# Kernel optimization log

Hardware: AMD Instinct MI355X
Metric: run time of the kernel (lower is better)

The kernel has to match this reference:

```python
import jax, jax.numpy as jnp
import numpy as np

B, DIM, HID = 16384, 1024, 2048
HALF = DIM // 2
# alternating checkerboard mask: even indices are 'masked' (conditioning) dims
_MASK = np.arange(DIM) % 2 == 0
MASK_IDX = np.nonzero(_MASK)[0]      # dims fed to the MLP (static)
NEG_IDX = np.nonzero(~_MASK)[0]      # dims transformed by the affine coupling (static)


def setup_inputs() -> dict:
    key = jax.random.key(0)
    ks = jax.random.split(key, 8)
    s = 0.02  # small init so exp(s) stays well-behaved
    return {
        "z": jax.random.normal(ks[0], (B, DIM), jnp.float32),
        "log_det": jnp.zeros((B,), jnp.float32),
        "W1": jax.random.normal(ks[1], (HID, HALF), jnp.float32) * s,
        "b1": jax.random.normal(ks[2], (HID,), jnp.float32) * s,
        "W2": jax.random.normal(ks[3], (HID, HID), jnp.float32) * s,
        "b2": jax.random.normal(ks[4], (HID,), jnp.float32) * s,
        "W3": jax.random.normal(ks[5], (DIM, HID), jnp.float32) * s,
        "b3": jax.random.normal(ks[6], (DIM,), jnp.float32) * s,
    }


def reference(z, log_det, W1, b1, W2, b2, W3, b3):
    # gather conditioning dims (static column indices -> jit-friendly)
    zm = z[:, MASK_IDX]                                    # [B, HALF]
    # 3-layer MLP with exact (erf) GELU, matching torch nn.GELU default
    h = jax.nn.gelu(zm @ W1.T + b1, approximate=False)     # [B, HID]
    h = jax.nn.gelu(h @ W2.T + b2, approximate=False)      # [B, HID]
    s_t = h @ W3.T + b3                                    # [B, DIM]
    s, t = s_t[:, :HALF], s_t[:, HALF:]                    # each [B, HALF]
    # affine coupling on the complementary dims, scatter back (forward, inverse=False)
    z_out = z.at[:, NEG_IDX].set(z[:, NEG_IDX] * jnp.exp(s) + t)
    log_det_out = log_det + jnp.sum(s, axis=1)
    return z_out, log_det_out
```

## Files before the change

kernel.cpp:

```cpp
#include <hip/hip_runtime.h>
#include <hip/hip_bf16.h>
#include <cstdint>

typedef __bf16 bf16x8 __attribute__((ext_vector_type(8)));
typedef float  f32x4  __attribute__((ext_vector_type(4)));

struct alignas(4) us2 { unsigned short x, y; };
struct alignas(8) us4 { unsigned short x, y, z, w; };

__device__ __forceinline__ unsigned short f2bf(float f) {
    union { float f; unsigned u; } a; a.f = f;
    unsigned r = a.u + 0x7fffu + ((a.u >> 16) & 1u);
    return (unsigned short)(r >> 16);
}

__device__ __forceinline__ void gl_lds16(const void* g, void* s) {
    __builtin_amdgcn_global_load_lds(
        (const __attribute__((address_space(1))) void*)g,
        (__attribute__((address_space(3))) void*)s, 16, 0, 0);
}

#define SCHEDB()  __builtin_amdgcn_sched_barrier(0)
#define SBAR()    do { SCHEDB(); __builtin_amdgcn_s_barrier(); SCHEDB(); } while (0)
#define WAITLG(N) do { asm volatile("s_waitcnt lgkmcnt(" #N ")" ::: "memory"); SCHEDB(); } while (0)
#define WAITVM(N) do { asm volatile("s_waitcnt vmcnt(" #N ")" ::: "memory"); SCHEDB(); } while (0)

template<int EPI, int K, int N>
__global__ __launch_bounds__(512, 2)
void gemm256(const unsigned short* __restrict__ A,
             const unsigned short* __restrict__ W,
             const float* __restrict__ bias,
             unsigned short* __restrict__ outb,
             float* __restrict__ outf,
             const float* __restrict__ zin,
             float* __restrict__ ldout)
{
    extern __shared__ char smem[];
    constexpr int NH = K / 32;
    constexpr int GX = N / 256;
    static_assert(NH % 2 == 0, "ping-pong unroll");

    const int tid  = threadIdx.x;
    const int lane = tid & 63;
    const int wv   = tid >> 6;
    const int wr   = wv >> 2, wc = wv & 3;

    const int bid = blockIdx.y * GX + blockIdx.x;
    const int nwg = GX * (int)gridDim.y;
    const int swz = (bid & 7) * (nwg >> 3) + (bid >> 3);
    const size_t row0 = (size_t)(swz / GX) * 256;
    const size_t col0 = (size_t)(swz % GX) * 256;

    const int cse = (((tid & 3) ^ ((tid >> 3) & 3)) << 3);
    const unsigned short* ag = A + (row0 + (tid >> 2)) * (size_t)K + cse;
    const unsigned short* bg = W + (col0 + (tid >> 2)) * (size_t)K + cse;

    auto stage = [&](int hh) {
        char* dA = smem + (hh & 3) * 16384 + tid * 16;
        char* dB = dA + 65536;
        const unsigned short* a = ag + (size_t)hh * 32;
        const unsigned short* b = bg + (size_t)hh * 32;
        gl_lds16(a,                     dA);
        gl_lds16(a + (size_t)128 * K,   dA + 8192);
        gl_lds16(b,                     dB);
        gl_lds16(b + (size_t)128 * K,   dB + 8192);
    };

    const int ln15 = lane & 15;
    const int xo   = (((lane >> 4) ^ ((ln15 >> 1) & 3)) << 4);
    const int arow = wr * 128 + ln15;
    const int brow = wc * 64 + ln15;

#define LD(base, row) (*(const bf16x8*)((base) + (size_t)(row) * 64 + xo))

    f32x4 acc[8][4] = {};
    bf16x8 A0[4], B0[4], A1[4], B1[4], aH[4];

    stage(0); stage(1); stage(2);
    WAITVM(8);
    SBAR();
#pragma unroll
    for (int mf = 0; mf < 4; ++mf) A0[mf] = LD(smem, arow + mf * 16);
#pragma unroll
    for (int nf = 0; nf < 4; ++nf) B0[nf] = LD(smem + 65536, brow + nf * 16);

    auto half_body = [&](int h, bf16x8 (&pA)[4], bf16x8 (&pB)[4],
                         bf16x8 (&nA)[4], bf16x8 (&nB)[4]) {
        const char* cA  = smem + (h & 3) * 16384;
        const char* cB  = cA + 65536;
        const char* cAn = smem + ((h + 1) & 3) * 16384;
        const char* cBn = cAn + 65536;

        if (h <= NH - 3) WAITVM(4);
        else             WAITVM(0);
        SBAR();

#pragma unroll
        for (int mf = 0; mf < 4; ++mf) aH[mf] = LD(cA, arow + 64 + mf * 16);
        WAITLG(4);
        __builtin_amdgcn_s_setprio(1);
#pragma unroll
        for (int mf = 0; mf < 4; ++mf)
#pragma unroll
            for (int nf = 0; nf < 4; ++nf)
                acc[mf][nf] = __builtin_amdgcn_mfma_f32_16x16x32_bf16(
                    pA[mf], pB[nf], acc[mf][nf], 0, 0, 0);
        __builtin_amdgcn_s_setprio(0);

        if (h + 1 < NH) {
#pragma unroll
            for (int mf = 0; mf < 4; ++mf) nA[mf] = LD(cAn, arow + mf * 16);
#pragma unroll
            for (int nf = 0; nf < 4; ++nf) nB[nf] = LD(cBn, brow + nf * 16);
            SCHEDB();
        }
        if (h + 3 < NH) stage(h + 3);

        if (h + 1 < NH) WAITLG(8);
        else            WAITLG(0);
        __builtin_amdgcn_s_setprio(1);
#pragma unroll
        for (int mf = 0; mf < 4; ++mf)
#pragma unroll
            for (int nf = 0; nf < 4; ++nf)
                acc[mf + 4][nf] = __builtin_amdgcn_mfma_f32_16x16x32_bf16(
                    aH[mf], pB[nf], acc[mf + 4][nf], 0, 0, 0);
        __builtin_amdgcn_s_setprio(0);
    };

    for (int h = 0; h < NH; h += 2) {
        half_body(h,     A0, B0, A1, B1);
        half_body(h + 1, A1, B1, A0, B0);
    }
#undef LD

    const int lq = lane >> 4;
    float bv[4];
#pragma unroll
    for (int nf = 0; nf < 4; ++nf) bv[nf] = bias[col0 + wc * 64 + nf * 16 + ln15];

    if (EPI == 2) {
        const float2* zin2 = (const float2*)zin;
        float2*       out2 = (float2*)outf;
#pragma unroll
        for (int mi = 0; mi < 8; ++mi) {
#pragma unroll
            for (int r = 0; r < 4; ++r) {
                const size_t row = row0 + wr * 128 + mi * 16 + lq * 4 + r;
                float sv = 0.f;
#pragma unroll
                for (int p = 0; p < 2; ++p) {
                    float s = acc[mi][2 * p][r] + bv[2 * p];
                    float t = acc[mi][2 * p + 1][r] + bv[2 * p + 1];
                    const size_t j = (col0 >> 1) + wc * 32 + p * 16 + ln15;
                    float2 zv = zin2[row * 512 + j];
                    float2 o; o.x = zv.x; o.y = zv.y * __expf(s) + t;
                    out2[row * 512 + j] = o;
                    sv += s;
                }
                sv += __shfl_xor(sv, 1, 64);
                sv += __shfl_xor(sv, 2, 64);
                sv += __shfl_xor(sv, 4, 64);
                sv += __shfl_xor(sv, 8, 64);
                if (ln15 == 0) atomicAdd(&ldout[row], sv);
            }
        }
    } else {
#pragma unroll
        for (int mi = 0; mi < 8; ++mi) {
#pragma unroll
            for (int r = 0; r < 4; ++r) {
                const size_t row = row0 + wr * 128 + mi * 16 + lq * 4 + r;
#pragma unroll
                for (int nf = 0; nf < 4; ++nf) {
                    const size_t col = col0 + wc * 64 + nf * 16 + ln15;
                    float v = acc[mi][nf][r] + bv[nf];
                    if (EPI == 0) {
                        float g = 0.5f * v * (1.0f + erff(v * 0.70710678118654752f));
                        outb[row * N + col] = f2bf(g);
                    } else {
                        outf[row * N + col] = v;
                    }
                }
            }
        }
    }
}

__global__ void prep_all(const float* __restrict__ W1, const float* __restrict__ W2,
                         const float* __restrict__ W3, const float* __restrict__ b3,
                         const float* __restrict__ z,  const float* __restrict__ ld,
                         unsigned short* __restrict__ w1b, unsigned short* __restrict__ w2b,
                         unsigned short* __restrict__ w3i, float* __restrict__ b3i,
                         unsigned short* __restrict__ zm,  float* __restrict__ ldout)
{
    constexpr int N1 = 2048 * 512 / 4;
    constexpr int N2 = 2048 * 2048 / 4;
    constexpr int N3 = 1024 * 2048 / 4;
    constexpr int N4 = 16384 * 1024 / 4;
    constexpr int N5 = 1024;
    constexpr int N6 = 16384;
    constexpr int TOT = N1 + N2 + N3 + N4 + N5 + N6;
    const int stride = gridDim.x * blockDim.x;
    for (int i = blockIdx.x * blockDim.x + threadIdx.x; i < TOT; i += stride) {
        int j = i;
        if (j < N1) {
            float4 v = ((const float4*)W1)[j];
            ((us4*)w1b)[j] = us4{ f2bf(v.x), f2bf(v.y), f2bf(v.z), f2bf(v.w) };
            continue;
        }
        j -= N1;
        if (j < N2) {
            float4 v = ((const float4*)W2)[j];
            ((us4*)w2b)[j] = us4{ f2bf(v.x), f2bf(v.y), f2bf(v.z), f2bf(v.w) };
            continue;
        }
        j -= N2;
        if (j < N3) {
            int row = j >> 9, c4 = j & 511;
            int q = row >> 5, u = row & 31;
            int srcrow = (u < 16) ? (q * 16 + u) : (512 + q * 16 + u - 16);
            float4 v = ((const float4*)W3)[(size_t)srcrow * 512 + c4];
            ((us4*)w3i)[j] = us4{ f2bf(v.x), f2bf(v.y), f2bf(v.z), f2bf(v.w) };
            continue;
        }
        j -= N3;
        if (j < N4) {
            float4 v = ((const float4*)z)[j];
            ((us2*)zm)[j] = us2{ f2bf(v.x), f2bf(v.z) };
            continue;
        }
        j -= N4;
        if (j < N5) {
            int q = j >> 5, u = j & 31;
            b3i[j] = b3[(u < 16) ? (q * 16 + u) : (512 + q * 16 + u - 16)];
            continue;
        }
        j -= N5;
        ldout[j] = ld[j];
    }
}

extern "C" void kernel_launch(void* const* d_in, const int* in_sizes, int n_in,
                              void* d_out, int out_size, void* d_ws, size_t ws_size,
                              hipStream_t stream)
{
    const float* z  = (const float*)d_in[0];
    const float* ld = (const float*)d_in[1];
    const float* W1 = (const float*)d_in[2];
    const float* b1 = (const float*)d_in[3];
    const float* W2 = (const float*)d_in[4];
    const float* b2 = (const float*)d_in[5];
    const float* W3 = (const float*)d_in[6];
    const float* b3 = (const float*)d_in[7];

    float* out   = (float*)d_out;
    float* zout  = out;
    float* ldout = out + (size_t)16384 * 1024;

    char* w = (char*)d_ws;
    unsigned short* zm  = (unsigned short*)w; w += (size_t)16384 * 512 * 2;
    unsigned short* w1b = (unsigned short*)w; w += (size_t)2048 * 512 * 2;
    unsigned short* w2b = (unsigned short*)w; w += (size_t)2048 * 2048 * 2;
    unsigned short* w3i = (unsigned short*)w; w += (size_t)1024 * 2048 * 2;
    unsigned short* h1  = (unsigned short*)w; w += (size_t)16384 * 2048 * 2;
    unsigned short* h2  = (unsigned short*)w; w += (size_t)16384 * 2048 * 2;
    float*          b3i = (float*)w;          w += 1024 * 4;

    (void)hipFuncSetAttribute((const void*)&gemm256<0, 512,  2048>,
                              hipFuncAttributeMaxDynamicSharedMemorySize, 131072);
    (void)hipFuncSetAttribute((const void*)&gemm256<0, 2048, 2048>,
                              hipFuncAttributeMaxDynamicSharedMemorySize, 131072);
    (void)hipFuncSetAttribute((const void*)&gemm256<2, 2048, 1024>,
                              hipFuncAttributeMaxDynamicSharedMemorySize, 131072);

    prep_all<<<2048, 256, 0, stream>>>(W1, W2, W3, b3, z, ld,
                                       w1b, w2b, w3i, b3i, zm, ldout);

    gemm256<0, 512,  2048><<<dim3(8, 64), 512, 131072, stream>>>(zm, w1b, b1, h1, nullptr, nullptr, nullptr);
    gemm256<0, 2048, 2048><<<dim3(8, 64), 512, 131072, stream>>>(h1, w2b, b2, h2, nullptr, nullptr, nullptr);
    gemm256<2, 2048, 1024><<<dim3(4, 64), 512, 131072, stream>>>(h2, w3i, b3i, nullptr, zout, z, ldout);
}
```

Baseline: 316.1 us.

## Switch GEMM inner loop to 32x32x16 bf16 MFMA tiles

Replaces the 16x16x32 MFMA fragments with 32x32x16 MFMA, which changes the LDS fragment loads, the K-split within each 32-wide stage, the accumulator layout and both epilogues. The W3/b3 interleave in prep is widened from 16 to 32 so that each wave's s/t pairs still line up. The aim is fewer MFMA issues and fewer LDS reads per unit of work, since larger tiles give more operand reuse. The trade-off is larger accumulator vectors and a different LDS access pattern that may cause bank conflicts, and the swizzle correctness with xo0^32 is subtle.

```diff
diff --git a/kernel.cpp b/kernel.cpp
--- a/kernel.cpp
+++ b/kernel.cpp
@@ -2,8 +2,8 @@
 #include <hip/hip_bf16.h>
 #include <cstdint>
 
-typedef __bf16 bf16x8 __attribute__((ext_vector_type(8)));
-typedef float  f32x4  __attribute__((ext_vector_type(4)));
+typedef __bf16 bf16x8  __attribute__((ext_vector_type(8)));
+typedef float  f32x16  __attribute__((ext_vector_type(16)));
 
 struct alignas(4) us2 { unsigned short x, y; };
 struct alignas(8) us4 { unsigned short x, y, z, w; };
@@ -38,7 +38,6 @@
     extern __shared__ char smem[];
     constexpr int NH = K / 32;
     constexpr int GX = N / 256;
-    static_assert(NH % 2 == 0, "ping-pong unroll");
 
     const int tid  = threadIdx.x;
     const int lane = tid & 63;
@@ -66,26 +65,26 @@
         gl_lds16(b + (size_t)128 * K,   dB + 8192);
     };
 
-    const int ln15 = lane & 15;
-    const int xo   = (((lane >> 4) ^ ((ln15 >> 1) & 3)) << 4);
-    const int arow = wr * 128 + ln15;
-    const int brow = wc * 64 + ln15;
-
-#define LD(base, row) (*(const bf16x8*)((base) + (size_t)(row) * 64 + xo))
-
-    f32x4 acc[8][4] = {};
-    bf16x8 A0[4], B0[4], A1[4], B1[4], aH[4];
+    const int ln31 = lane & 31;
+    const int khi  = lane >> 5;
+    const int xo0  = (((khi) ^ ((ln31 >> 1) & 3)) << 4);
+    const int arow = wr * 128 + ln31;
+    const int brow = wc * 64 + ln31;
+
+#define LD32(base, rowb, X) (*(const bf16x8*)((base) + (size_t)(rowb) * 64 + (xo0 ^ (X))))
+
+    f32x16 acc[4][2] = {};
+    bf16x8 F0[6], F1[6];
 
     stage(0); stage(1); stage(2);
     WAITVM(8);
     SBAR();
 #pragma unroll
-    for (int mf = 0; mf < 4; ++mf) A0[mf] = LD(smem, arow + mf * 16);
-#pragma unroll
-    for (int nf = 0; nf < 4; ++nf) B0[nf] = LD(smem + 65536, brow + nf * 16);
-
-    auto half_body = [&](int h, bf16x8 (&pA)[4], bf16x8 (&pB)[4],
-                         bf16x8 (&nA)[4], bf16x8 (&nB)[4]) {
+    for (int mf = 0; mf < 4; ++mf) F0[mf] = LD32(smem, arow + mf * 32, 0);
+#pragma unroll
+    for (int nf = 0; nf < 2; ++nf) F0[4 + nf] = LD32(smem + 65536, brow + nf * 32, 0);
+
+    auto half_body = [&](int h, bf16x8 (&pF)[6], bf16x8 (&nF)[6]) {
         const char* cA  = smem + (h & 3) * 16384;
         const char* cB  = cA + 65536;
         const char* cAn = smem + ((h + 1) & 3) * 16384;
@@ -95,86 +94,88 @@
         else             WAITVM(0);
         SBAR();
 
-#pragma unroll
-        for (int mf = 0; mf < 4; ++mf) aH[mf] = LD(cA, arow + 64 + mf * 16);
-        WAITLG(4);
+        bf16x8 cF[6];
+#pragma unroll
+        for (int mf = 0; mf < 4; ++mf) cF[mf] = LD32(cA, arow + mf * 32, 32);
+#pragma unroll
+        for (int nf = 0; nf < 2; ++nf) cF[4 + nf] = LD32(cB, brow + nf * 32, 32);
+
+        WAITLG(6);
         __builtin_amdgcn_s_setprio(1);
 #pragma unroll
         for (int mf = 0; mf < 4; ++mf)
 #pragma unroll
-            for (int nf = 0; nf < 4; ++nf)
-                acc[mf][nf] = __builtin_amdgcn_mfma_f32_16x16x32_bf16(
-                    pA[mf], pB[nf], acc[mf][nf], 0, 0, 0);
+            for (int nf = 0; nf < 2; ++nf)
+                acc[mf][nf] = __builtin_amdgcn_mfma_f32_32x32x16_bf16(
+                    pF[mf], pF[4 + nf], acc[mf][nf], 0, 0, 0);
         __builtin_amdgcn_s_setprio(0);
 
         if (h + 1 < NH) {
 #pragma unroll
-            for (int mf = 0; mf < 4; ++mf) nA[mf] = LD(cAn, arow + mf * 16);
-#pragma unroll
-            for (int nf = 0; nf < 4; ++nf) nB[nf] = LD(cBn, brow + nf * 16);
+            for (int mf = 0; mf < 4; ++mf) nF[mf] = LD32(cAn, arow + mf * 32, 0);
+#pragma unroll
+            for (int nf = 0; nf < 2; ++nf) nF[4 + nf] = LD32(cBn, brow + nf * 32, 0);
             SCHEDB();
         }
         if (h + 3 < NH) stage(h + 3);
 
-        if (h + 1 < NH) WAITLG(8);
+        if (h + 1 < NH) WAITLG(6);
         else            WAITLG(0);
         __builtin_amdgcn_s_setprio(1);
 #pragma unroll
         for (int mf = 0; mf < 4; ++mf)
 #pragma unroll
-            for (int nf = 0; nf < 4; ++nf)
-                acc[mf + 4][nf] = __builtin_amdgcn_mfma_f32_16x16x32_bf16(
-                    aH[mf], pB[nf], acc[mf + 4][nf], 0, 0, 0);
+            for (int nf = 0; nf < 2; ++nf)
+                acc[mf][nf] = __builtin_amdgcn_mfma_f32_32x32x16_bf16(
+                    cF[mf], cF[4 + nf], acc[mf][nf], 0, 0, 0);
         __builtin_amdgcn_s_setprio(0);
     };
 
     for (int h = 0; h < NH; h += 2) {
-        half_body(h,     A0, B0, A1, B1);
-        half_body(h + 1, A1, B1, A0, B0);
+        half_body(h,     F0, F1);
+        half_body(h + 1, F1, F0);
     }
-#undef LD
-
-    const int lq = lane >> 4;
-    float bv[4];
-#pragma unroll
-    for (int nf = 0; nf < 4; ++nf) bv[nf] = bias[col0 + wc * 64 + nf * 16 + ln15];
+#undef LD32
+
+    float bv[2];
+#pragma unroll
+    for (int nf = 0; nf < 2; ++nf) bv[nf] = bias[col0 + wc * 64 + nf * 32 + ln31];
 
     if (EPI == 2) {
         const float2* zin2 = (const float2*)zin;
         float2*       out2 = (float2*)outf;
-#pragma unroll
-        for (int mi = 0; mi < 8; ++mi) {
-#pragma unroll
-            for (int r = 0; r < 4; ++r) {
-                const size_t row = row0 + wr * 128 + mi * 16 + lq * 4 + r;
-                float sv = 0.f;
-#pragma unroll
-                for (int p = 0; p < 2; ++p) {
-                    float s = acc[mi][2 * p][r] + bv[2 * p];
-                    float t = acc[mi][2 * p + 1][r] + bv[2 * p + 1];
-                    const size_t j = (col0 >> 1) + wc * 32 + p * 16 + ln15;
-                    float2 zv = zin2[row * 512 + j];
-                    float2 o; o.x = zv.x; o.y = zv.y * __expf(s) + t;
-                    out2[row * 512 + j] = o;
-                    sv += s;
-                }
+        const size_t jj = (col0 >> 1) + wc * 32 + ln31;
+#pragma unroll
+        for (int mf = 0; mf < 4; ++mf) {
+#pragma unroll
+            for (int r = 0; r < 16; ++r) {
+                const size_t row = row0 + wr * 128 + mf * 32
+                                 + (r & 3) + 8 * (r >> 2) + 4 * khi;
+                float s = acc[mf][0][r] + bv[0];
+                float t = acc[mf][1][r] + bv[1];
+                float2 zv = zin2[row * 512 + jj];
+                float2 o; o.x = zv.x; o.y = zv.y * __expf(s) + t;
+                out2[row * 512 + jj] = o;
+                float sv = s;
                 sv += __shfl_xor(sv, 1, 64);
                 sv += __shfl_xor(sv, 2, 64);
                 sv += __shfl_xor(sv, 4, 64);
                 sv += __shfl_xor(sv, 8, 64);
-                if (ln15 == 0) atomicAdd(&ldout[row], sv);
+                sv += __shfl_xor(sv, 16, 64);
+                if (ln31 == 0) atomicAdd(&ldout[row], sv);
             }
         }
     } else {
 #pragma unroll
-        for (int mi = 0; mi < 8; ++mi) {
-#pragma unroll
-            for (int r = 0; r < 4; ++r) {
-                const size_t row = row0 + wr * 128 + mi * 16 + lq * 4 + r;
-#pragma unroll
-                for (int nf = 0; nf < 4; ++nf) {
-                    const size_t col = col0 + wc * 64 + nf * 16 + ln15;
-                    float v = acc[mi][nf][r] + bv[nf];
+        for (int mf = 0; mf < 4; ++mf) {
+#pragma unroll
+            for (int r = 0; r < 16; ++r) {
+                const size_t row = row0 + wr * 128 + mf * 32
+                                 + (r & 3) + 8 * (r >> 2) + 4 * khi;
+#pragma unroll
+                for (int nf = 0; nf < 2; ++nf) {
+                    const size_t col = col0 + wc * 64 + nf * 32 + ln31;
+                    float v = acc[mf][nf][r] + bv[nf];
                     if (EPI == 0) {
                         float g = 0.5f * v * (1.0f + erff(v * 0.70710678118654752f));
                         outb[row * N + col] = f2bf(g);
@@ -218,8 +219,8 @@
         j -= N2;
         if (j < N3) {
             int row = j >> 9, c4 = j & 511;
-            int q = row >> 5, u = row & 31;
-            int srcrow = (u < 16) ? (q * 16 + u) : (512 + q * 16 + u - 16);
+            int q = row >> 6, u = row & 63;
+            int srcrow = (u < 32) ? (q * 32 + u) : (512 + q * 32 + u - 32);
             float4 v = ((const float4*)W3)[(size_t)srcrow * 512 + c4];
             ((us4*)w3i)[j] = us4{ f2bf(v.x), f2bf(v.y), f2bf(v.z), f2bf(v.w) };
             continue;
@@ -232,8 +233,8 @@
         }
         j -= N4;
         if (j < N5) {
-            int q = j >> 5, u = j & 31;
-            b3i[j] = b3[(u < 16) ? (q * 16 + u) : (512 + q * 16 + u - 16)];
+            int q = j >> 6, u = j & 63;
+            b3i[j] = b3[(u < 32) ? (q * 32 + u) : (512 + q * 32 + u - 32)];
             continue;
         }
         j -= N5;
```

Result: slower. 354.5 us (+12.2%).
